# Performance work log

Measured on AMD Instinct MI355X. Metric: run time of the kernel, lower is better.

## Reference

```python
import jax, jax.numpy as jnp
import numpy as np
from jax import lax

H, W, C, HIDDEN = 1024, 1024, 16, 128

_SOBEL_X = jnp.array([[-1., 0., 1.], [-2., 0., 2.], [-1., 0., 1.]], dtype=jnp.float32)
_SOBEL_Y = jnp.array([[-1., -2., -1.], [0., 0., 0.], [1., 2., 1.]], dtype=jnp.float32)


def setup_inputs() -> dict:
    key = jax.random.key(0)
    ks = jax.random.split(key, 5)
    state = jax.random.normal(ks[0], (H, W, C), dtype=jnp.float32)
    # 1x1 convs are per-pixel matmuls; expose weights as (out,in) matrices.
    # NOTE: the torch module zero-inits the output layer; we randomize for a
    # non-trivial numerical baseline.
    W1 = jax.random.normal(ks[1], (HIDDEN, 3 * C), dtype=jnp.float32) * 0.1
    b1 = jax.random.normal(ks[2], (HIDDEN,), dtype=jnp.float32) * 0.1
    W2 = jax.random.normal(ks[3], (C, HIDDEN), dtype=jnp.float32) * 0.1
    b2 = jax.random.normal(ks[4], (C,), dtype=jnp.float32) * 0.1
    return {"state": state, "W1": W1, "b1": b1, "W2": W2, "b2": b2}


def _depthwise_circular(x, k2d):
    # x: (1, C, H, W); k2d: (3, 3). Circular pad then VALID depthwise conv
    # (torch Conv2d is cross-correlation, matching lax.conv_general_dilated).
    c = x.shape[1]
    xp = jnp.pad(x, ((0, 0), (0, 0), (1, 1), (1, 1)), mode="wrap")
    kern = jnp.broadcast_to(k2d, (c, 1, 3, 3))  # (O=C, I/groups=1, 3, 3)
    return lax.conv_general_dilated(
        xp, kern, window_strides=(1, 1), padding="VALID",
        dimension_numbers=("NCHW", "OIHW", "NCHW"), feature_group_count=c)


def reference(state, W1, b1, W2, b2):
    # state: (H, W, C) -> (1, C, H, W)
    x = jnp.transpose(state, (2, 0, 1))[None]
    gx = _depthwise_circular(x, _SOBEL_X)
    gy = _depthwise_circular(x, _SOBEL_Y)
    perc = jnp.concatenate([gx, gy, x], axis=1)  # (1, 3C, H, W)
    hidden = jax.nn.relu(
        jnp.einsum("oc,bchw->bohw", W1, perc) + b1[None, :, None, None])
    delta = jnp.einsum("co,bohw->bchw", W2, hidden) + b2[None, :, None, None]
    return jnp.transpose(delta[0], (1, 2, 0))  # (H, W, C)
```

## Files before the change

kernel.cpp:

```cpp
#include <hip/hip_runtime.h>


constexpr int Hc = 1024, Wc = 1024;
constexpr int W1S = 152;
constexpr int W1PAD = 19968;

typedef __attribute__((ext_vector_type(8))) short short8;
typedef __attribute__((ext_vector_type(4))) float f32x4;
typedef __attribute__((ext_vector_type(2))) unsigned int uint2v;

__device__ __forceinline__ unsigned short bfu(float x) {
    __bf16 b = (__bf16)x;
    return __builtin_bit_cast(unsigned short, b);
}
__device__ __forceinline__ unsigned pack2(float a, float b) {
    return (unsigned)bfu(a) | ((unsigned)bfu(b) << 16);
}

__device__ __forceinline__ void swap32(unsigned x, unsigned y, unsigned& o0, unsigned& o1) {
#if __has_builtin(__builtin_amdgcn_permlane32_swap)
    uint2v r = __builtin_amdgcn_permlane32_swap(x, y, false, false);
    o0 = r[0]; o1 = r[1];
#else
    unsigned xs = (unsigned)__shfl_xor((int)x, 32, 64);
    unsigned ys = (unsigned)__shfl_xor((int)y, 32, 64);
    const bool hi = (threadIdx.x & 32) != 0;
    o0 = hi ? ys : x;
    o1 = hi ? y : xs;
#endif
}
__device__ __forceinline__ void swap16(unsigned a, unsigned b, unsigned& o0, unsigned& o1) {
#if __has_builtin(__builtin_amdgcn_permlane16_swap)
    uint2v r = __builtin_amdgcn_permlane16_swap(a, b, false, false);
    o0 = r[0]; o1 = r[1];
#else
    unsigned as = (unsigned)__shfl_xor((int)a, 16, 64);
    unsigned bs = (unsigned)__shfl_xor((int)b, 16, 64);
    const bool hi = (threadIdx.x & 16) != 0;
    o0 = hi ? bs : a;
    o1 = hi ? b : as;
#endif
}

__global__ __launch_bounds__(256) void nca_prep(
    const float* __restrict__ W1c, const float* __restrict__ b1c,
    const float* __restrict__ W2c,
    unsigned short* __restrict__ ws1, unsigned short* __restrict__ ws2)
{
    const int u = blockIdx.x * 256 + threadIdx.x;
    if (u < W1PAD) {
        const int row = u / W1S, k = u - row * W1S;
        float v = 0.f;
        if (row < 128) {
            if (k < 144) {
                const int pos = k >> 4, c = k & 15;
                const int dy = pos / 3, dx = pos - dy * 3;
                v = (float)((dx - 1) * (1 + (dy == 1))) * W1c[row * 48 + c]
                  + (float)((dy - 1) * (1 + (dx == 1))) * W1c[row * 48 + 16 + c];
                if (pos == 4) v += W1c[row * 48 + 32 + c];
            } else if (k == 144) {
                v = b1c[row];
            }
        }
        ws1[u] = bfu(v);
    } else if (u < W1PAD + 16 * 128) {
        const int w = u - W1PAD;
        ws2[w] = bfu(W2c[w]);
    }
}

template <bool USE_WS>
__global__ __launch_bounds__(256, 2) void nca_main(
    const float* __restrict__ state,
    const float* __restrict__ W1c, const float* __restrict__ b1c,
    const float* __restrict__ W2c, const float* __restrict__ b2c,
    const unsigned short* __restrict__ ws1,
    const unsigned short* __restrict__ ws2,
    float* __restrict__ out)
{
    __shared__ short w1f[W1PAD];
    __shared__ short tile[6 * 66 * 16];

    const int tid  = threadIdx.x;
    const int lane = tid & 63;
    const int wv   = tid >> 6;
    const int p    = lane & 15;
    const int g    = lane >> 4;

    const int bid = (int)blockIdx.x;
    const int r0 = (bid >> 4) << 4;
    const int c0 = (bid & 15) << 6;

    if (USE_WS) {
        #pragma unroll
        for (int it = 0; it < 10; ++it) {
            const int chunk = it * 4 + wv;
            if (chunk < 39) {
                const int off = chunk * 1024;
                __builtin_amdgcn_global_load_lds(
                    (const __attribute__((address_space(1))) unsigned int*)
                        ((const char*)ws1 + off + lane * 16),
                    (__attribute__((address_space(3))) unsigned int*)
                        ((char*)w1f + off),
                    16, 0, 0);
            }
        }
    } else {
        for (int u = tid; u < W1PAD; u += 256) {
            const int row = u / W1S, k = u - row * W1S;
            float v = 0.f;
            if (row < 128) {
                if (k < 144) {
                    const int pos = k >> 4, c = k & 15;
                    const int dy = pos / 3, dx = pos - dy * 3;
                    v = (float)((dx - 1) * (1 + (dy == 1))) * W1c[row * 48 + c]
                      + (float)((dy - 1) * (1 + (dx == 1))) * W1c[row * 48 + 16 + c];
                    if (pos == 4) v += W1c[row * 48 + 32 + c];
                } else if (k == 144) {
                    v = b1c[row];
                }
            }
            w1f[u] = (short)bfu(v);
        }
    }

    int grow[4], gcol[4], lofs[4];
    #pragma unroll
    for (int s = 0; s < 4; ++s) {
        const int j = tid + 256 * s;
        const int jj = (j < 792) ? j : 791;
        const int pidx = jj >> 1, hb = jj & 1;
        const int tr = pidx / 66, tc = pidx - tr * 66;
        grow[s] = tr;
        gcol[s] = (((c0 - 1 + tc) & (Wc - 1)) << 6) + (hb << 5);
        lofs[s] = (jj * 16) ^ ((jj & 8) << 1);
    }
    const bool has3 = (tid < 24);

    short8 w2f[4];
    if (USE_WS) {
        const unsigned short* wsp = ws2 + p * 128 + 8 * g;
        #pragma unroll
        for (int kc = 0; kc < 4; ++kc)
            w2f[kc] = *reinterpret_cast<const short8*>(wsp + 32 * kc);
    } else {
        #pragma unroll
        for (int kc = 0; kc < 4; ++kc) {
            const float* qp = W2c + p * 128 + 32 * kc + 8 * g;
            const float4 A = *reinterpret_cast<const float4*>(qp);
            const float4 B = *reinterpret_cast<const float4*>(qp + 4);
            uint4 uu{pack2(A.x, A.y), pack2(A.z, A.w), pack2(B.x, B.y), pack2(B.z, B.w)};
            w2f[kc] = __builtin_bit_cast(short8, uu);
        }
    }
    const float4 bv = *reinterpret_cast<const float4*>(b2c + 4 * g);

    const int gb = g & 1;
    int baddr[5];
    #pragma unroll
    for (int i = 0; i < 5; ++i) {
        const int pos = (i < 4) ? (2 * i + (g >> 1)) : 8;
        const int dy = pos / 3, dx = pos - 3 * dy;
        const int pidx = (wv + dy) * 66 + (p + dx);
        baddr[i] = (pidx * 32 + gb * 16) ^ ((pidx & 4) << 2);
    }
    const int abase = p * W1S + 8 * g;

    int ocol[4];
    #pragma unroll
    for (int pt = 0; pt < 4; ++pt) ocol[pt] = ((c0 + 16 * pt + p) << 6) + (g << 4);

    const char* stby = (const char*)state;
    const char* tby  = (const char*)tile;
    char* outby = (char*)out;

    {
        float4 sa[4], sb[4];
        #pragma unroll
        for (int s = 0; s < 4; ++s) {
            if (s < 3 || has3) {
                const long sr = (long)((r0 - 1 + grow[s]) & (Hc - 1));
                const char* bp = stby + (sr << 16) + gcol[s];
                sa[s] = *reinterpret_cast<const float4*>(bp);
                sb[s] = *reinterpret_cast<const float4*>(bp + 16);
            }
        }
        #pragma unroll
        for (int s = 0; s < 4; ++s) {
            if (s < 3 || has3) {
                uint4 uu{pack2(sa[s].x, sa[s].y), pack2(sa[s].z, sa[s].w),
                         pack2(sb[s].x, sb[s].y), pack2(sb[s].z, sb[s].w)};
                *reinterpret_cast<uint4*>((char*)tile + lofs[s]) = uu;
            }
        }
    }
    __syncthreads();

    #pragma unroll 1
    for (int t = 0; t < 4; ++t) {
        f32x4 acc2[4];
        #pragma unroll
        for (int pt = 0; pt < 4; ++pt) {
            acc2[pt][0] = bv.x; acc2[pt][1] = bv.y; acc2[pt][2] = bv.z; acc2[pt][3] = bv.w;
        }

        #pragma unroll
        for (int half = 0; half < 2; ++half) {
            short8 Ar[4][5];
            #pragma unroll
            for (int tt = 0; tt < 4; ++tt) {
                #pragma unroll
                for (int i = 0; i < 5; ++i) {
                    Ar[tt][i] = *reinterpret_cast<const short8*>(
                        &w1f[abase + (64 * half + 16 * tt) * W1S + 32 * i]);
                }
            }

            __builtin_amdgcn_s_setprio(1);
            #pragma unroll
            for (int pt = 0; pt < 4; ++pt) {
                short8 bf[5];
                #pragma unroll
                for (int i = 0; i < 5; ++i) {
                    if (i < 4) {
                        bf[i] = *reinterpret_cast<const short8*>(tby + baddr[i] + pt * 512);
                    } else {
                        if (g < 2) {
                            bf[i] = *reinterpret_cast<const short8*>(tby + baddr[4] + pt * 512);
                        } else if (g == 2) {
                            uint4 uu{0x3F80u, 0u, 0u, 0u};
                            bf[i] = __builtin_bit_cast(short8, uu);
                        } else {
                            uint4 uu{0u, 0u, 0u, 0u};
                            bf[i] = __builtin_bit_cast(short8, uu);
                        }
                    }
                }

                f32x4 h[4];
                #pragma unroll
                for (int tt = 0; tt < 4; ++tt) h[tt] = (f32x4){0.f, 0.f, 0.f, 0.f};
                #pragma unroll
                for (int i = 0; i < 5; ++i) {
                    #pragma unroll
                    for (int tt = 0; tt < 4; ++tt)
                        h[tt] = __builtin_amdgcn_mfma_f32_16x16x32_bf16(Ar[tt][i], bf[i], h[tt], 0, 0, 0);
                }

                #pragma unroll
                for (int pr = 0; pr < 2; ++pr) {
                    const f32x4 ha = h[2 * pr], hc = h[2 * pr + 1];
                    const unsigned Pa0 = pack2(fmaxf(ha[0], 0.f), fmaxf(ha[1], 0.f));
                    const unsigned Pa1 = pack2(fmaxf(ha[2], 0.f), fmaxf(ha[3], 0.f));
                    const unsigned Pb0 = pack2(fmaxf(hc[0], 0.f), fmaxf(hc[1], 0.f));
                    const unsigned Pb1 = pack2(fmaxf(hc[2], 0.f), fmaxf(hc[3], 0.f));
                    unsigned s0, s1, t0, t1, u0, u1, u2, u3;
                    swap32(Pa0, Pb0, s0, s1);
                    swap16(s0, s1, u0, u2);
                    swap32(Pa1, Pb1, t0, t1);
                    swap16(t0, t1, u1, u3);
                    uint4 uu{u0, u1, u2, u3};
                    acc2[pt] = __builtin_amdgcn_mfma_f32_16x16x32_bf16(
                        w2f[2 * half + pr], __builtin_bit_cast(short8, uu), acc2[pt], 0, 0, 0);
                }
            }
            __builtin_amdgcn_s_setprio(0);
        }

        float4 sa[4], sb[4];
        if (t < 3) {
            const int rb = r0 + 4 * (t + 1) - 1;
            #pragma unroll
            for (int s = 0; s < 4; ++s) {
                if (s < 3 || has3) {
                    const long sr = (long)((rb + grow[s]) & (Hc - 1));
                    const char* bp = stby + (sr << 16) + gcol[s];
                    sa[s] = *reinterpret_cast<const float4*>(bp);
                    sb[s] = *reinterpret_cast<const float4*>(bp + 16);
                }
            }
        }

        const long orow = (long)(r0 + 4 * t + wv) << 16;
        #pragma unroll
        for (int pt = 0; pt < 4; ++pt) {
            float4 o; o.x = acc2[pt][0]; o.y = acc2[pt][1]; o.z = acc2[pt][2]; o.w = acc2[pt][3];
            *reinterpret_cast<float4*>(outby + orow + ocol[pt]) = o;
        }

        if (t < 3) {
            __syncthreads();
            #pragma unroll
            for (int s = 0; s < 4; ++s) {
                if (s < 3 || has3) {
                    uint4 uu{pack2(sa[s].x, sa[s].y), pack2(sa[s].z, sa[s].w),
                             pack2(sb[s].x, sb[s].y), pack2(sb[s].z, sb[s].w)};
                    *reinterpret_cast<uint4*>((char*)tile + lofs[s]) = uu;
                }
            }
            __syncthreads();
        }
    }
}

extern "C" void kernel_launch(void* const* d_in, const int* in_sizes, int n_in,
                              void* d_out, int out_size, void* d_ws, size_t ws_size,
                              hipStream_t stream) {
    const float* state = (const float*)d_in[0];
    const float* W1c   = (const float*)d_in[1];
    const float* b1c   = (const float*)d_in[2];
    const float* W2c   = (const float*)d_in[3];
    const float* b2c   = (const float*)d_in[4];
    float* out = (float*)d_out;

    unsigned short* ws1 = (unsigned short*)d_ws;
    unsigned short* ws2 = ws1 + W1PAD;
    const size_t ws_needed = (size_t)(W1PAD + 16 * 128) * sizeof(unsigned short);

    if (ws_size >= ws_needed) {
        nca_prep<<<(W1PAD + 16 * 128 + 255) / 256, 256, 0, stream>>>(W1c, b1c, W2c, ws1, ws2);
        nca_main<true><<<1024, 256, 0, stream>>>(state, W1c, b1c, W2c, b2c, ws1, ws2, out);
    } else {
        nca_main<false><<<1024, 256, 0, stream>>>(state, W1c, b1c, W2c, b2c, ws1, ws2, out);
    }
}
```

Baseline: 76.37 us.

## Double-buffer state tile and read W1 fragments directly from global

Measured after the change: 128.5 us. 68.2% more time.

```diff
diff --git a/kernel.cpp b/kernel.cpp
--- a/kernel.cpp
+++ b/kernel.cpp
@@ -4,6 +4,7 @@
 constexpr int Hc = 1024, Wc = 1024;
 constexpr int W1S = 152;
 constexpr int W1PAD = 19968;
+constexpr int TBUF = 6 * 66 * 16;
 
 typedef __attribute__((ext_vector_type(8))) short short8;
 typedef __attribute__((ext_vector_type(4))) float f32x4;
@@ -78,8 +79,8 @@
     const unsigned short* __restrict__ ws2,
     float* __restrict__ out)
 {
-    __shared__ short w1f[W1PAD];
-    __shared__ short tile[6 * 66 * 16];
+    __shared__ short tile[2][TBUF];
+    __shared__ short w1f[USE_WS ? 16 : W1PAD];
 
     const int tid  = threadIdx.x;
     const int lane = tid & 63;
@@ -91,21 +92,7 @@
     const int r0 = (bid >> 4) << 4;
     const int c0 = (bid & 15) << 6;
 
-    if (USE_WS) {
-        #pragma unroll
-        for (int it = 0; it < 10; ++it) {
-            const int chunk = it * 4 + wv;
-            if (chunk < 39) {
-                const int off = chunk * 1024;
-                __builtin_amdgcn_global_load_lds(
-                    (const __attribute__((address_space(1))) unsigned int*)
-                        ((const char*)ws1 + off + lane * 16),
-                    (__attribute__((address_space(3))) unsigned int*)
-                        ((char*)w1f + off),
-                    16, 0, 0);
-            }
-        }
-    } else {
+    if constexpr (!USE_WS) {
         for (int u = tid; u < W1PAD; u += 256) {
             const int row = u / W1S, k = u - row * W1S;
             float v = 0.f;
@@ -171,7 +158,6 @@
     for (int pt = 0; pt < 4; ++pt) ocol[pt] = ((c0 + 16 * pt + p) << 6) + (g << 4);
 
     const char* stby = (const char*)state;
-    const char* tby  = (const char*)tile;
     char* outby = (char*)out;
 
     {
@@ -190,7 +176,7 @@
             if (s < 3 || has3) {
                 uint4 uu{pack2(sa[s].x, sa[s].y), pack2(sa[s].z, sa[s].w),
                          pack2(sb[s].x, sb[s].y), pack2(sb[s].z, sb[s].w)};
-                *reinterpret_cast<uint4*>((char*)tile + lofs[s]) = uu;
+                *reinterpret_cast<uint4*>((char*)&tile[0][0] + lofs[s]) = uu;
             }
         }
     }
@@ -198,6 +184,21 @@
 
     #pragma unroll 1
     for (int t = 0; t < 4; ++t) {
+        float4 sa[4], sb[4];
+        if (t < 3) {
+            const int rb = r0 + 4 * (t + 1) - 1;
+            #pragma unroll
+            for (int s = 0; s < 4; ++s) {
+                if (s < 3 || has3) {
+                    const long sr = (long)((rb + grow[s]) & (Hc - 1));
+                    const char* bp = stby + (sr << 16) + gcol[s];
+                    sa[s] = *reinterpret_cast<const float4*>(bp);
+                    sb[s] = *reinterpret_cast<const float4*>(bp + 16);
+                }
+            }
+        }
+
+        const char* tby = (const char*)&tile[t & 1][0];
         f32x4 acc2[4];
         #pragma unroll
         for (int pt = 0; pt < 4; ++pt) {
@@ -211,8 +212,11 @@
             for (int tt = 0; tt < 4; ++tt) {
                 #pragma unroll
                 for (int i = 0; i < 5; ++i) {
-                    Ar[tt][i] = *reinterpret_cast<const short8*>(
-                        &w1f[abase + (64 * half + 16 * tt) * W1S + 32 * i]);
+                    const int ofs = abase + (64 * half + 16 * tt) * W1S + 32 * i;
+                    if constexpr (USE_WS)
+                        Ar[tt][i] = *reinterpret_cast<const short8*>(ws1 + ofs);
+                    else
+                        Ar[tt][i] = *reinterpret_cast<const short8*>(&w1f[ofs]);
                 }
             }
 
@@ -267,20 +271,6 @@
             __builtin_amdgcn_s_setprio(0);
         }
 
-        float4 sa[4], sb[4];
-        if (t < 3) {
-            const int rb = r0 + 4 * (t + 1) - 1;
-            #pragma unroll
-            for (int s = 0; s < 4; ++s) {
-                if (s < 3 || has3) {
-                    const long sr = (long)((rb + grow[s]) & (Hc - 1));
-                    const char* bp = stby + (sr << 16) + gcol[s];
-                    sa[s] = *reinterpret_cast<const float4*>(bp);
-                    sb[s] = *reinterpret_cast<const float4*>(bp + 16);
-                }
-            }
-        }
-
         const long orow = (long)(r0 + 4 * t + wv) << 16;
         #pragma unroll
         for (int pt = 0; pt < 4; ++pt) {
@@ -289,13 +279,13 @@
         }
 
         if (t < 3) {
-            __syncthreads();
+            char* wb = (char*)&tile[(t + 1) & 1][0];
             #pragma unroll
             for (int s = 0; s < 4; ++s) {
                 if (s < 3 || has3) {
                     uint4 uu{pack2(sa[s].x, sa[s].y), pack2(sa[s].z, sa[s].w),
                              pack2(sb[s].x, sb[s].y), pack2(sb[s].z, sb[s].w)};
-                    *reinterpret_cast<uint4*>((char*)tile + lofs[s]) = uu;
+                    *reinterpret_cast<uint4*>(wb + lofs[s]) = uu;
                 }
             }
             __syncthreads();
```

## Give each wave a private row ring buffer and pre-swizzle W1 into MFMA fragments

Applied to the files above, without the earlier changes.

Measured after the change: 68.97 us. 1.11x faster.

```diff
diff --git a/kernel.cpp b/kernel.cpp
--- a/kernel.cpp
+++ b/kernel.cpp
@@ -2,8 +2,8 @@
 
 
 constexpr int Hc = 1024, Wc = 1024;
-constexpr int W1S = 152;
-constexpr int W1PAD = 19968;
+constexpr int W1FRAG = 20480;
+constexpr int RSTRIDE = 2112;
 
 typedef __attribute__((ext_vector_type(8))) short short8;
 typedef __attribute__((ext_vector_type(4))) float f32x4;
@@ -42,29 +42,36 @@
 #endif
 }
 
+__device__ __forceinline__ float w1fold_val(
+    const float* __restrict__ W1c, const float* __restrict__ b1c, int row, int k)
+{
+    if (k < 144) {
+        const int pos = k >> 4, c = k & 15;
+        const int dy = pos / 3, dx = pos - dy * 3;
+        float v = (float)((dx - 1) * (1 + (dy == 1))) * W1c[row * 48 + c]
+                + (float)((dy - 1) * (1 + (dx == 1))) * W1c[row * 48 + 16 + c];
+        if (pos == 4) v += W1c[row * 48 + 32 + c];
+        return v;
+    }
+    return (k == 144) ? b1c[row] : 0.f;
+}
+
 __global__ __launch_bounds__(256) void nca_prep(
     const float* __restrict__ W1c, const float* __restrict__ b1c,
     const float* __restrict__ W2c,
     unsigned short* __restrict__ ws1, unsigned short* __restrict__ ws2)
 {
     const int u = blockIdx.x * 256 + threadIdx.x;
-    if (u < W1PAD) {
-        const int row = u / W1S, k = u - row * W1S;
-        float v = 0.f;
-        if (row < 128) {
-            if (k < 144) {
-                const int pos = k >> 4, c = k & 15;
-                const int dy = pos / 3, dx = pos - dy * 3;
-                v = (float)((dx - 1) * (1 + (dy == 1))) * W1c[row * 48 + c]
-                  + (float)((dy - 1) * (1 + (dx == 1))) * W1c[row * 48 + 16 + c];
-                if (pos == 4) v += W1c[row * 48 + 32 + c];
-            } else if (k == 144) {
-                v = b1c[row];
-            }
-        }
-        ws1[u] = bfu(v);
-    } else if (u < W1PAD + 16 * 128) {
-        const int w = u - W1PAD;
+    if (u < W1FRAG) {
+        const int j = u >> 9, w = u & 511;
+        const int l = w >> 3, e = w & 7;
+        const int half = j / 20, rem = j - half * 20;
+        const int tt = rem / 5, i = rem - tt * 5;
+        const int row = (l & 15) + 16 * tt + 64 * half;
+        const int k = 32 * i + 8 * (l >> 4) + e;
+        ws1[u] = bfu(w1fold_val(W1c, b1c, row, k));
+    } else if (u < W1FRAG + 16 * 128) {
+        const int w = u - W1FRAG;
         ws2[w] = bfu(W2c[w]);
     }
 }
@@ -78,8 +85,8 @@
     const unsigned short* __restrict__ ws2,
     float* __restrict__ out)
 {
-    __shared__ short w1f[W1PAD];
-    __shared__ short tile[6 * 66 * 16];
+    __shared__ short w1f[W1FRAG];
+    __shared__ short ring[4][4][RSTRIDE / 2];
 
     const int tid  = threadIdx.x;
     const int lane = tid & 63;
@@ -90,52 +97,31 @@
     const int bid = (int)blockIdx.x;
     const int r0 = (bid >> 4) << 4;
     const int c0 = (bid & 15) << 6;
+    const int x0 = r0 + 4 * wv;
 
     if (USE_WS) {
         #pragma unroll
         for (int it = 0; it < 10; ++it) {
             const int chunk = it * 4 + wv;
-            if (chunk < 39) {
-                const int off = chunk * 1024;
-                __builtin_amdgcn_global_load_lds(
-                    (const __attribute__((address_space(1))) unsigned int*)
-                        ((const char*)ws1 + off + lane * 16),
-                    (__attribute__((address_space(3))) unsigned int*)
-                        ((char*)w1f + off),
-                    16, 0, 0);
-            }
+            const int off = chunk * 1024;
+            __builtin_amdgcn_global_load_lds(
+                (const __attribute__((address_space(1))) unsigned int*)
+                    ((const char*)ws1 + off + lane * 16),
+                (__attribute__((address_space(3))) unsigned int*)
+                    ((char*)w1f + off),
+                16, 0, 0);
         }
     } else {
-        for (int u = tid; u < W1PAD; u += 256) {
-            const int row = u / W1S, k = u - row * W1S;
-            float v = 0.f;
-            if (row < 128) {
-                if (k < 144) {
-                    const int pos = k >> 4, c = k & 15;
-                    const int dy = pos / 3, dx = pos - dy * 3;
-                    v = (float)((dx - 1) * (1 + (dy == 1))) * W1c[row * 48 + c]
-                      + (float)((dy - 1) * (1 + (dx == 1))) * W1c[row * 48 + 16 + c];
-                    if (pos == 4) v += W1c[row * 48 + 32 + c];
-                } else if (k == 144) {
-                    v = b1c[row];
-                }
-            }
-            w1f[u] = (short)bfu(v);
-        }
-    }
-
-    int grow[4], gcol[4], lofs[4];
-    #pragma unroll
-    for (int s = 0; s < 4; ++s) {
-        const int j = tid + 256 * s;
-        const int jj = (j < 792) ? j : 791;
-        const int pidx = jj >> 1, hb = jj & 1;
-        const int tr = pidx / 66, tc = pidx - tr * 66;
-        grow[s] = tr;
-        gcol[s] = (((c0 - 1 + tc) & (Wc - 1)) << 6) + (hb << 5);
-        lofs[s] = (jj * 16) ^ ((jj & 8) << 1);
-    }
-    const bool has3 = (tid < 24);
+        for (int u = tid; u < W1FRAG; u += 256) {
+            const int j = u >> 9, w = u & 511;
+            const int l = w >> 3, e = w & 7;
+            const int half = j / 20, rem = j - half * 20;
+            const int tt = rem / 5, i = rem - tt * 5;
+            const int row = (l & 15) + 16 * tt + 64 * half;
+            const int k = 32 * i + 8 * (l >> 4) + e;
+            w1f[u] = (short)bfu(w1fold_val(W1c, b1c, row, k));
+        }
+    }
 
     short8 w2f[4];
     if (USE_WS) {
@@ -156,48 +142,93 @@
     const float4 bv = *reinterpret_cast<const float4*>(b2c + 4 * g);
 
     const int gb = g & 1;
-    int baddr[5];
+    int dyi[5], colb[5];
     #pragma unroll
     for (int i = 0; i < 5; ++i) {
         const int pos = (i < 4) ? (2 * i + (g >> 1)) : 8;
         const int dy = pos / 3, dx = pos - 3 * dy;
-        const int pidx = (wv + dy) * 66 + (p + dx);
-        baddr[i] = (pidx * 32 + gb * 16) ^ ((pidx & 4) << 2);
-    }
-    const int abase = p * W1S + 8 * g;
+        dyi[i] = dy;
+        const int tc = p + dx;
+        colb[i] = (tc * 32 + gb * 16) ^ ((tc & 4) << 2);
+    }
+
+    int sgc[5], swb[5];
+    #pragma unroll
+    for (int s = 0; s < 5; ++s) {
+        const int ch = (s < 4) ? (lane + 64 * s) : (256 + lane);
+        const int tc = ch >> 2, q = ch & 3;
+        sgc[s] = (((c0 - 1 + tc) & (Wc - 1)) << 6) + (q << 4);
+        swb[s] = (tc * 32 + q * 8) ^ ((tc & 4) << 2);
+    }
+    const bool has4 = (lane < 8);
 
     int ocol[4];
     #pragma unroll
     for (int pt = 0; pt < 4; ++pt) ocol[pt] = ((c0 + 16 * pt + p) << 6) + (g << 4);
 
     const char* stby = (const char*)state;
-    const char* tby  = (const char*)tile;
+    char* ringw = (char*)&ring[wv][0][0];
     char* outby = (char*)out;
 
-    {
-        float4 sa[4], sb[4];
-        #pragma unroll
-        for (int s = 0; s < 4; ++s) {
-            if (s < 3 || has3) {
-                const long sr = (long)((r0 - 1 + grow[s]) & (Hc - 1));
-                const char* bp = stby + (sr << 16) + gcol[s];
-                sa[s] = *reinterpret_cast<const float4*>(bp);
-                sb[s] = *reinterpret_cast<const float4*>(bp + 16);
+    #pragma unroll
+    for (int d = 0; d < 3; ++d) {
+        const long gr = (long)((x0 - 1 + d) & (Hc - 1)) << 16;
+        const int slot = ((x0 - 1 + d) & 3) * RSTRIDE;
+        float4 sr5[5];
+        #pragma unroll
+        for (int s = 0; s < 5; ++s)
+            if (s < 4 || has4)
+                sr5[s] = *reinterpret_cast<const float4*>(stby + gr + sgc[s]);
+        #pragma unroll
+        for (int s = 0; s < 5; ++s)
+            if (s < 4 || has4) {
+                uint2 pk; pk.x = pack2(sr5[s].x, sr5[s].y); pk.y = pack2(sr5[s].z, sr5[s].w);
+                *reinterpret_cast<uint2*>(ringw + slot + swb[s]) = pk;
             }
-        }
-        #pragma unroll
-        for (int s = 0; s < 4; ++s) {
-            if (s < 3 || has3) {
-                uint4 uu{pack2(sa[s].x, sa[s].y), pack2(sa[s].z, sa[s].w),
-                         pack2(sb[s].x, sb[s].y), pack2(sb[s].z, sb[s].w)};
-                *reinterpret_cast<uint4*>((char*)tile + lofs[s]) = uu;
-            }
-        }
-    }
+    }
+
     __syncthreads();
 
     #pragma unroll 1
     for (int t = 0; t < 4; ++t) {
+        const int x = x0 + t;
+
+        float4 sr5[5];
+        if (t < 3) {
+            const long gr = (long)((x + 2) & (Hc - 1)) << 16;
+            #pragma unroll
+            for (int s = 0; s < 5; ++s)
+                if (s < 4 || has4)
+                    sr5[s] = *reinterpret_cast<const float4*>(stby + gr + sgc[s]);
+        }
+
+        int sb[5];
+        #pragma unroll
+        for (int i = 0; i < 5; ++i) sb[i] = ((x - 1 + dyi[i]) & 3) * RSTRIDE;
+
+        short8 bfa[4][5];
+        #pragma unroll
+        for (int pt = 0; pt < 4; ++pt) {
+            #pragma unroll
+            for (int i = 0; i < 5; ++i) {
+                if (i < 4) {
+                    bfa[pt][i] = *reinterpret_cast<const short8*>(
+                        ringw + sb[i] + colb[i] + pt * 512);
+                } else {
+                    if (g < 2) {
+                        bfa[pt][i] = *reinterpret_cast<const short8*>(
+                            ringw + sb[4] + colb[4] + pt * 512);
+                    } else if (g == 2) {
+                        uint4 uu{0x3F80u, 0u, 0u, 0u};
+                        bfa[pt][i] = __builtin_bit_cast(short8, uu);
+                    } else {
+                        uint4 uu{0u, 0u, 0u, 0u};
+                        bfa[pt][i] = __builtin_bit_cast(short8, uu);
+                    }
+                }
+            }
+        }
+
         f32x4 acc2[4];
         #pragma unroll
         for (int pt = 0; pt < 4; ++pt) {
@@ -211,32 +242,15 @@
             for (int tt = 0; tt < 4; ++tt) {
                 #pragma unroll
                 for (int i = 0; i < 5; ++i) {
+                    const int j = (half * 4 + tt) * 5 + i;
                     Ar[tt][i] = *reinterpret_cast<const short8*>(
-                        &w1f[abase + (64 * half + 16 * tt) * W1S + 32 * i]);
+                        (char*)w1f + j * 1024 + lane * 16);
                 }
             }
 
             __builtin_amdgcn_s_setprio(1);
             #pragma unroll
             for (int pt = 0; pt < 4; ++pt) {
-                short8 bf[5];
-                #pragma unroll
-                for (int i = 0; i < 5; ++i) {
-                    if (i < 4) {
-                        bf[i] = *reinterpret_cast<const short8*>(tby + baddr[i] + pt * 512);
-                    } else {
-                        if (g < 2) {
-                            bf[i] = *reinterpret_cast<const short8*>(tby + baddr[4] + pt * 512);
-                        } else if (g == 2) {
-                            uint4 uu{0x3F80u, 0u, 0u, 0u};
-                            bf[i] = __builtin_bit_cast(short8, uu);
-                        } else {
-                            uint4 uu{0u, 0u, 0u, 0u};
-                            bf[i] = __builtin_bit_cast(short8, uu);
-                        }
-                    }
-                }
-
                 f32x4 h[4];
                 #pragma unroll
                 for (int tt = 0; tt < 4; ++tt) h[tt] = (f32x4){0.f, 0.f, 0.f, 0.f};
@@ -244,7 +258,8 @@
                 for (int i = 0; i < 5; ++i) {
                     #pragma unroll
                     for (int tt = 0; tt < 4; ++tt)
-                        h[tt] = __builtin_amdgcn_mfma_f32_16x16x32_bf16(Ar[tt][i], bf[i], h[tt], 0, 0, 0);
+                        h[tt] = __builtin_amdgcn_mfma_f32_16x16x32_bf16(
+                            Ar[tt][i], bfa[pt][i], h[tt], 0, 0, 0);
                 }
 
                 #pragma unroll
@@ -267,21 +282,7 @@
             __builtin_amdgcn_s_setprio(0);
         }
 
-        float4 sa[4], sb[4];
-        if (t < 3) {
-            const int rb = r0 + 4 * (t + 1) - 1;
-            #pragma unroll
-            for (int s = 0; s < 4; ++s) {
-                if (s < 3 || has3) {
-                    const long sr = (long)((rb + grow[s]) & (Hc - 1));
-                    const char* bp = stby + (sr << 16) + gcol[s];
-                    sa[s] = *reinterpret_cast<const float4*>(bp);
-                    sb[s] = *reinterpret_cast<const float4*>(bp + 16);
-                }
-            }
-        }
-
-        const long orow = (long)(r0 + 4 * t + wv) << 16;
+        const long orow = (long)x << 16;
         #pragma unroll
         for (int pt = 0; pt < 4; ++pt) {
             float4 o; o.x = acc2[pt][0]; o.y = acc2[pt][1]; o.z = acc2[pt][2]; o.w = acc2[pt][3];
@@ -289,16 +290,13 @@
         }
 
         if (t < 3) {
-            __syncthreads();
-            #pragma unroll
-            for (int s = 0; s < 4; ++s) {
-                if (s < 3 || has3) {
-                    uint4 uu{pack2(sa[s].x, sa[s].y), pack2(sa[s].z, sa[s].w),
-                             pack2(sb[s].x, sb[s].y), pack2(sb[s].z, sb[s].w)};
-                    *reinterpret_cast<uint4*>((char*)tile + lofs[s]) = uu;
-                }
-            }
-            __syncthreads();
+            const int slot = ((x + 2) & 3) * RSTRIDE;
+            #pragma unroll
+            for (int s = 0; s < 5; ++s)
+                if (s < 4 || has4) {
+                    uint2 pk; pk.x = pack2(sr5[s].x, sr5[s].y); pk.y = pack2(sr5[s].z, sr5[s].w);
+                    *reinterpret_cast<uint2*>(ringw + slot + swb[s]) = pk;
+                }
         }
     }
 }
@@ -314,11 +312,11 @@
     float* out = (float*)d_out;
 
     unsigned short* ws1 = (unsigned short*)d_ws;
-    unsigned short* ws2 = ws1 + W1PAD;
-    const size_t ws_needed = (size_t)(W1PAD + 16 * 128) * sizeof(unsigned short);
+    unsigned short* ws2 = ws1 + W1FRAG;
+    const size_t ws_needed = (size_t)(W1FRAG + 16 * 128) * sizeof(unsigned short);
 
     if (ws_size >= ws_needed) {
-        nca_prep<<<(W1PAD + 16 * 128 + 255) / 256, 256, 0, stream>>>(W1c, b1c, W2c, ws1, ws2);
+        nca_prep<<<(W1FRAG + 16 * 128 + 255) / 256, 256, 0, stream>>>(W1c, b1c, W2c, ws1, ws2);
         nca_main<true><<<1024, 256, 0, stream>>>(state, W1c, b1c, W2c, b2c, ws1, ws2, out);
     } else {
         nca_main<false><<<1024, 256, 0, stream>>>(state, W1c, b1c, W2c, b2c, ws1, ws2, out);
```
